# Optimization experiments

Hardware: AMD Instinct MI355X
Metric: run time of the kernel (lower is better)

The kernel has to match this reference:

```python
import jax, jax.numpy as jnp
import numpy as np

B, T, D, H, C = 128, 1000, 40, 128, 8  # batch, time, input feats, hidden, classes


def _lstm_layer(x, Wih, Whh, bih, bhh):
    """Unidirectional LSTM over time. x: [B,T,Din] -> [B,T,H]. PyTorch gate order i,f,g,o."""
    Bn = x.shape[0]
    Hn = Whh.shape[1]
    b = bih + bhh
    def step(carry, xt):
        h, c = carry
        g = xt @ Wih.T + h @ Whh.T + b  # [B,4H]
        i, f, gg, o = jnp.split(g, 4, axis=-1)
        c = jax.nn.sigmoid(f) * c + jax.nn.sigmoid(i) * jnp.tanh(gg)
        h = jax.nn.sigmoid(o) * jnp.tanh(c)
        return (h, c), h
    h0 = jnp.zeros((Bn, Hn), x.dtype)
    _, hs = jax.lax.scan(step, (h0, h0), jnp.swapaxes(x, 0, 1))  # scan over time
    return jnp.swapaxes(hs, 0, 1)


def _bilstm_layer(x, pf, pb):
    fwd = _lstm_layer(x, *pf)
    bwd = jnp.flip(_lstm_layer(jnp.flip(x, 1), *pb), 1)
    return jnp.concatenate([fwd, bwd], axis=-1)  # [B,T,2H]


def setup_inputs() -> dict:
    key = jax.random.key(0)
    ks = jax.random.split(key, 16)
    s = 0.05
    def rn(k, shape):
        return jax.random.normal(k, shape, jnp.float32) * s
    inp = {"x": jax.random.normal(ks[0], (B, T, D), jnp.float32)}
    inp["ln_g"] = jnp.ones((D,), jnp.float32)
    inp["ln_b"] = jnp.zeros((D,), jnp.float32)
    dims = [D, 2 * H]  # layer-0 input feats, layer-1 input feats
    i = 1
    for l in range(2):
        for d in ("f", "b"):
            inp[f"Wih_{d}{l}"] = rn(ks[i], (4 * H, dims[l])); i += 1
            inp[f"Whh_{d}{l}"] = rn(ks[i], (4 * H, H)); i += 1
            inp[f"bih_{d}{l}"] = jnp.zeros((4 * H,), jnp.float32)
            inp[f"bhh_{d}{l}"] = jnp.zeros((4 * H,), jnp.float32)
    inp["attn_W1"] = rn(ks[i], (H, 2 * H)); i += 1
    inp["attn_b1"] = jnp.zeros((H,), jnp.float32)
    inp["attn_w2"] = rn(ks[i], (1, H)); i += 1
    inp["fc_W1"] = rn(ks[i], (H, 2 * H)); i += 1
    inp["fc_b1"] = jnp.zeros((H,), jnp.float32)
    inp["fc_W2"] = rn(ks[i], (C, H)); i += 1
    inp["fc_b2"] = jnp.zeros((C,), jnp.float32)
    return inp


def reference(x, ln_g, ln_b,
              Wih_f0, Whh_f0, bih_f0, bhh_f0, Wih_b0, Whh_b0, bih_b0, bhh_b0,
              Wih_f1, Whh_f1, bih_f1, bhh_f1, Wih_b1, Whh_b1, bih_b1, bhh_b1,
              attn_W1, attn_b1, attn_w2, fc_W1, fc_b1, fc_W2, fc_b2):
    # LayerNorm over feature dim (eps=1e-5, PyTorch default)
    mu = jnp.mean(x, axis=-1, keepdims=True)
    var = jnp.var(x, axis=-1, keepdims=True)
    xn = (x - mu) * jax.lax.rsqrt(var + 1e-5) * ln_g + ln_b
    # 2-layer bidirectional LSTM
    h = _bilstm_layer(xn, (Wih_f0, Whh_f0, bih_f0, bhh_f0), (Wih_b0, Whh_b0, bih_b0, bhh_b0))
    h = _bilstm_layer(h, (Wih_f1, Whh_f1, bih_f1, bhh_f1), (Wih_b1, Whh_b1, bih_b1, bhh_b1))
    # attention pooling: Linear-Tanh-Linear(no bias) -> softmax over time
    scores = jnp.tanh(h @ attn_W1.T + attn_b1) @ attn_w2[0]  # [B,T]
    w = jax.nn.softmax(scores, axis=1)
    ctx = jnp.einsum('bt,btd->bd', w, h)  # [B,2H]
    # MLP classifier head
    hid = jax.nn.relu(ctx @ fc_W1.T + fc_b1)
    return hid @ fc_W2.T + fc_b2  # [B,C] logits
```

## Files before the change

### kernel.cpp

```cpp
#include <hip/hip_runtime.h>

#define T_ 1000

typedef float v2f __attribute__((ext_vector_type(2)));

__device__ __forceinline__ float sigf(float x) { return 1.0f / (1.0f + __expf(-x)); }
__device__ __forceinline__ float tanh_fast(float x) { return 1.0f - 2.0f / (1.0f + __expf(2.0f * x)); }
__device__ __forceinline__ float dot4(float4 a, float4 b) {
  return a.x * b.x + a.y * b.y + a.z * b.z + a.w * b.w;
}
__device__ __forceinline__ void pkfma(v2f& acc, float4 w, float4 v) {
  v2f wl; wl[0] = w.x; wl[1] = w.y;
  v2f wh; wh[0] = w.z; wh[1] = w.w;
  v2f vl; vl[0] = v.x; vl[1] = v.y;
  v2f vh; vh[0] = v.z; vh[1] = v.w;
  acc += wl * vl;
  acc += wh * vh;
}
__device__ __forceinline__ unsigned short f2bf(float f) {
  unsigned u = __float_as_uint(f);
  u = (u + 0x7fffu + ((u >> 16) & 1u)) >> 16;
  return (unsigned short)u;
}
__device__ __forceinline__ float bf2f(unsigned short h) {
  return __uint_as_float(((unsigned)h) << 16);
}
__device__ __forceinline__ float4 bf4_to_f4(ushort4 u) {
  float4 r;
  r.x = bf2f(u.x); r.y = bf2f(u.y); r.z = bf2f(u.z); r.w = bf2f(u.w);
  return r;
}

__global__ void bail_kernel(float* out, int n) {
  for (int i = threadIdx.x; i < n; i += 256) out[i] = 0.0f;
}

__global__ __launch_bounds__(256) void ln_stats_kernel(const float* __restrict__ x,
                                                       float* __restrict__ mu_arr,
                                                       float* __restrict__ rs_arr) {
  const int lane = threadIdx.x & 63;
  const int w = threadIdx.x >> 6;
  const long row = (long)blockIdx.x * 4 + w;
  float v = (lane < 40) ? x[row * 40 + lane] : 0.0f;
  float s1 = v, s2 = v * v;
  for (int m = 32; m; m >>= 1) {
    s1 += __shfl_xor(s1, m, 64);
    s2 += __shfl_xor(s2, m, 64);
  }
  if (lane == 0) {
    const float mu = s1 * (1.0f / 40.0f);
    const float var = s2 * (1.0f / 40.0f) - mu * mu;
    mu_arr[row] = mu;
    rs_arr[row] = rsqrtf(var + 1e-5f);
  }
}

__global__ __launch_bounds__(512, 1) void rec0_kernel(
    const float* __restrict__ x,
    const float* __restrict__ mu_arr, const float* __restrict__ rs_arr,
    const float* __restrict__ ln_g, const float* __restrict__ ln_b,
    const float* __restrict__ Wih_f, const float* __restrict__ Whh_f,
    const float* __restrict__ bih_f, const float* __restrict__ bhh_f,
    const float* __restrict__ Wih_b, const float* __restrict__ Whh_b,
    const float* __restrict__ bih_b, const float* __restrict__ bhh_b,
    float* __restrict__ h0) {
  const int tid = threadIdx.x;
  const int u = (tid >> 6) * 16 + ((tid & 63) >> 2);
  const int p = tid & 3;
  const int brow = blockIdx.x & 127;
  const int dir = blockIdx.x >> 7;
  const float* __restrict__ Wih = dir ? Wih_b : Wih_f;
  const float* __restrict__ Whh = dir ? Whh_b : Whh_f;
  const float* __restrict__ bih = dir ? bih_b : bih_f;
  const float* __restrict__ bhh = dir ? bhh_b : bhh_f;

  float4 wh[4][8];
  float4 wi[4][3];
  float S1[4], bias[4];
#pragma unroll
  for (int g = 0; g < 4; ++g) {
    const int row = g * 128 + u;
    const float4* wr = (const float4*)(Whh + row * 128 + p * 32);
#pragma unroll
    for (int ff = 0; ff < 8; ++ff) wh[g][ff] = wr[(ff + 2 * p) & 7];
    float s1p = 0.0f, s2p = 0.0f;
#pragma unroll
    for (int f = 0; f < 3; ++f) {
      float tmp[4];
#pragma unroll
      for (int e = 0; e < 4; ++e) {
        const int k = p * 12 + f * 4 + e;
        const float wv = (k < 40) ? Wih[row * 40 + k] : 0.0f;
        const float gk = (k < 40) ? ln_g[k] : 0.0f;
        const float bk = (k < 40) ? ln_b[k] : 0.0f;
        const float wf = wv * gk;
        tmp[e] = wf;
        s1p += wf;
        s2p += wv * bk;
      }
      wi[g][f] = make_float4(tmp[0], tmp[1], tmp[2], tmp[3]);
    }
    s1p += __shfl_xor(s1p, 1, 64); s1p += __shfl_xor(s1p, 2, 64);
    s2p += __shfl_xor(s2p, 1, 64); s2p += __shfl_xor(s2p, 2, 64);
    S1[g] = s1p;
    bias[g] = bih[g * 128 + u] + bhh[g * 128 + u] + s2p;
  }

  __shared__ float h4f[128];
  __shared__ __align__(16) float x_ring[2][8][48];
  __shared__ float mu_ring[2][8], rs_ring[2][8];
  __shared__ float hring[2][8][128];

  const int lr8 = tid / 40;
  const int lcol = tid - lr8 * 40;
  const long xbase = (long)brow * T_ * 40;
  const long mbase = (long)brow * T_;
  const long hbase = (long)brow * T_ * 256;

  if (tid < 128) h4f[tid] = 0.0f;
  if (tid < 128) {
    const int b = tid >> 6, r = (tid >> 3) & 7, cc = 40 + (tid & 7);
    x_ring[b][r][cc] = 0.0f;
  }
  if (tid < 320) {
    const int t = lr8;
    const int tt = dir ? (T_ - 1 - t) : t;
    x_ring[0][lr8][lcol] = x[xbase + (long)tt * 40 + lcol];
  } else if (tid < 328) {
    const int t = tid - 320;
    const int tt = dir ? (T_ - 1 - t) : t;
    mu_ring[0][t] = mu_arr[mbase + tt];
  } else if (tid < 336) {
    const int t = tid - 328;
    const int tt = dir ? (T_ - 1 - t) : t;
    rs_ring[0][t] = rs_arr[mbase + tt];
  }
  float c = 0.0f;
  float xpf = 0.0f, mupf = 0.0f, rspf = 0.0f;
  __syncthreads();

  for (int sb = 0; sb < 125; ++sb) {
    const int rb = sb & 1;
#pragma unroll
    for (int su = 0; su < 8; ++su) {
      if (su == 0) {
        if (sb + 1 < 125) {
          if (tid < 320) {
            const int t = (sb + 1) * 8 + lr8;
            const int tt = dir ? (T_ - 1 - t) : t;
            xpf = x[xbase + (long)tt * 40 + lcol];
          } else if (tid < 328) {
            const int t = (sb + 1) * 8 + (tid - 320);
            const int tt = dir ? (T_ - 1 - t) : t;
            mupf = mu_arr[mbase + tt];
          } else if (tid < 336) {
            const int t = (sb + 1) * 8 + (tid - 328);
            const int tt = dir ? (T_ - 1 - t) : t;
            rspf = rs_arr[mbase + tt];
          }
        }
        if (sb > 0) {
#pragma unroll
          for (int e = 0; e < 2; ++e) {
            const int idx = tid + e * 512;
            const int v = idx >> 7, j = idx & 127;
            const int ts = (sb - 1) * 8 + v;
            const int te = dir ? (T_ - 1 - ts) : ts;
            h0[hbase + (long)te * 256 + dir * 128 + j] = hring[rb ^ 1][v][j];
          }
        }
      }
      v2f hacc[4], xacc[4];
#pragma unroll
      for (int g = 0; g < 4; ++g) { hacc[g] = 0.0f; xacc[g] = 0.0f; }
      const float4* h4v = (const float4*)h4f;
#pragma unroll
      for (int ff = 0; ff < 8; ++ff) {
        const float4 hv = h4v[p * 8 + ((ff + 2 * p) & 7)];
        pkfma(hacc[0], wh[0][ff], hv);
        pkfma(hacc[1], wh[1][ff], hv);
        pkfma(hacc[2], wh[2][ff], hv);
        pkfma(hacc[3], wh[3][ff], hv);
      }
      const float4* xr4 = (const float4*)x_ring[rb][su];
#pragma unroll
      for (int f = 0; f < 3; ++f) {
        const float4 xv = xr4[p * 3 + f];
        pkfma(xacc[0], wi[0][f], xv);
        pkfma(xacc[1], wi[1][f], xv);
        pkfma(xacc[2], wi[2][f], xv);
        pkfma(xacc[3], wi[3][f], xv);
      }
      const float rs = rs_ring[rb][su];
      const float mu = mu_ring[rb][su];
      float pg[4];
#pragma unroll
      for (int g = 0; g < 4; ++g) {
        pg[g] = (hacc[g][0] + hacc[g][1]) + rs * (xacc[g][0] + xacc[g][1]);
        pg[g] += __shfl_xor(pg[g], 1, 64);
        pg[g] += __shfl_xor(pg[g], 2, 64);
        pg[g] += bias[g] - rs * mu * S1[g];
      }
      const float ig = sigf(pg[0]);
      const float fg = sigf(pg[1]);
      const float gg = tanh_fast(pg[2]);
      const float og = sigf(pg[3]);
      c = fg * c + ig * gg;
      const float hv = og * tanh_fast(c);
      if (p == 0) { h4f[u] = hv; hring[rb][su][u] = hv; }
      if (su == 7 && sb + 1 < 125) {
        if (tid < 320) x_ring[rb ^ 1][lr8][lcol] = xpf;
        else if (tid < 328) mu_ring[rb ^ 1][tid - 320] = mupf;
        else if (tid < 336) rs_ring[rb ^ 1][tid - 328] = rspf;
      }
      __syncthreads();
    }
  }
#pragma unroll
  for (int e = 0; e < 2; ++e) {
    const int idx = tid + e * 512;
    const int v = idx >> 7, j = idx & 127;
    const int ts = 124 * 8 + v;
    const int te = dir ? (T_ - 1 - ts) : ts;
    h0[hbase + (long)te * 256 + dir * 128 + j] = hring[0][v][j];
  }
}

__global__ __launch_bounds__(512, 1) void rec1_kernel(
    const float* __restrict__ xw_f, const float* __restrict__ xw_b,
    const float* __restrict__ Whh_f, const float* __restrict__ bih_f, const float* __restrict__ bhh_f,
    const float* __restrict__ Whh_b, const float* __restrict__ bih_b, const float* __restrict__ bhh_b,
    unsigned short* __restrict__ h1b, float* __restrict__ state,
    int Tc, int t0f, int t0b, int first) {
  const int tid = threadIdx.x;
  const int u = (tid >> 6) * 16 + ((tid & 63) >> 2);
  const int p = tid & 3;
  const int brow = blockIdx.x & 127;
  const int dir = blockIdx.x >> 7;
  const float* __restrict__ xw = dir ? xw_b : xw_f;
  const float* __restrict__ Whh = dir ? Whh_b : Whh_f;
  const float* __restrict__ bih = dir ? bih_b : bih_f;
  const float* __restrict__ bhh = dir ? bhh_b : bhh_f;
  const int t0 = dir ? t0b : t0f;

  float4 wh[4][8];
#pragma unroll
  for (int g = 0; g < 4; ++g) {
    const float4* wr = (const float4*)(Whh + (g * 128 + u) * 128 + p * 32);
#pragma unroll
    for (int ff = 0; ff < 8; ++ff) wh[g][ff] = wr[(ff + 2 * p) & 7];
  }
  const int myrow = p * 128 + u;
  const float bias_p = bih[myrow] + bhh[myrow];

  __shared__ float h4f[128];
  __shared__ float hring[2][8][128];
  float* sblk = state + (long)blockIdx.x * 256;
  float c = 0.0f;
  if (first) {
    if (tid < 128) h4f[tid] = 0.0f;
  } else {
    if (tid < 128) h4f[tid] = sblk[tid];
    c = sblk[128 + u];
  }
  const long gbase = (long)brow * Tc;
  float xr[8];
#pragma unroll
  for (int v = 0; v < 8; ++v) {
    xr[v] = 0.0f;
    if (v < Tc) {
      const int tr = dir ? (Tc - 1 - v) : v;
      xr[v] = xw[(gbase + tr) * 512 + myrow];
    }
  }
  __syncthreads();

  const int nSB = (Tc + 7) / 8;
  for (int sb = 0; sb < nSB; ++sb) {
    const int rb = sb & 1;
#pragma unroll
    for (int su = 0; su < 8; ++su) {
      const int s = sb * 8 + su;
      if (s >= Tc) break;
      if (su == 0 && sb > 0) {
#pragma unroll
        for (int e = 0; e < 2; ++e) {
          const int idx = tid + e * 512;
          const int v = idx >> 7, j = idx & 127;
          const int s2 = (sb - 1) * 8 + v;
          const int tt = dir ? (Tc - 1 - s2) : s2;
          h1b[((long)brow * T_ + (t0 + tt)) * 256 + dir * 128 + j] = f2bf(hring[rb ^ 1][v][j]);
        }
      }
      v2f hacc[4];
#pragma unroll
      for (int g = 0; g < 4; ++g) hacc[g] = 0.0f;
      const float4* h4v = (const float4*)h4f;
#pragma unroll
      for (int ff = 0; ff < 8; ++ff) {
        const float4 hv = h4v[p * 8 + ((ff + 2 * p) & 7)];
        pkfma(hacc[0], wh[0][ff], hv);
        pkfma(hacc[1], wh[1][ff], hv);
        pkfma(hacc[2], wh[2][ff], hv);
        pkfma(hacc[3], wh[3][ff], hv);
      }
      const float xin = xr[su] + bias_p;
      float pg[4];
#pragma unroll
      for (int g = 0; g < 4; ++g) {
        pg[g] = hacc[g][0] + hacc[g][1] + ((p == g) ? xin : 0.0f);
        pg[g] += __shfl_xor(pg[g], 1, 64);
        pg[g] += __shfl_xor(pg[g], 2, 64);
      }
      const float ig = sigf(pg[0]);
      const float fg = sigf(pg[1]);
      const float gg = tanh_fast(pg[2]);
      const float og = sigf(pg[3]);
      c = fg * c + ig * gg;
      const float hv = og * tanh_fast(c);
      if (p == 0) { h4f[u] = hv; hring[rb][su][u] = hv; }
      if (su == 7) {
#pragma unroll
        for (int v = 0; v < 8; ++v) {
          const int sn = s + 1 + v;
          xr[v] = 0.0f;
          if (sn < Tc) {
            const int tr = dir ? (Tc - 1 - sn) : sn;
            xr[v] = xw[(gbase + tr) * 512 + myrow];
          }
        }
      }
      __syncthreads();
    }
  }
  {
    const int sbL = (Tc - 1) >> 3;
    const int cnt = Tc - sbL * 8;
    const int rbL = sbL & 1;
#pragma unroll
    for (int e = 0; e < 2; ++e) {
      const int idx = tid + e * 512;
      const int v = idx >> 7, j = idx & 127;
      if (v < cnt) {
        const int s2 = sbL * 8 + v;
        const int tt = dir ? (Tc - 1 - s2) : s2;
        h1b[((long)brow * T_ + (t0 + tt)) * 256 + dir * 128 + j] = f2bf(hring[rbL][v][j]);
      }
    }
  }
  if (tid < 128) sblk[tid] = h4f[tid];
  if (p == 0) sblk[128 + u] = c;
}

__global__ __launch_bounds__(256, 2) void gemm_xw1(
    const float* __restrict__ h0,
    const float* __restrict__ Wf, const float* __restrict__ Wb,
    float* __restrict__ xwf, float* __restrict__ xwb,
    int Tc, int t0f, int t0b) {
  __shared__ float As[64 * 36];
  __shared__ float Bs[128 * 36];
  __shared__ int rowbase[64];
  const int tid = threadIdx.x;
  const int tx = tid & 15, ty = tid >> 4;
  const int r0 = blockIdx.x * 64;
  const int jt = blockIdx.y;
  const int dir = jt >> 2;
  const int nh = jt & 3;
  const float* __restrict__ W = dir ? Wb : Wf;
  float* __restrict__ out = dir ? xwb : xwf;
  const int jbase = nh * 128;
  const int t0 = dir ? t0b : t0f;

  if (tid < 64) {
    const int r = r0 + tid;
    const int br = r / Tc;
    rowbase[tid] = br * T_ + t0 + (r - br * Tc);
  }

  float4* As4 = (float4*)As;
  float4* Bs4 = (float4*)Bs;
  v2f acc2[4][8];
#pragma unroll
  for (int r = 0; r < 4; ++r)
#pragma unroll
    for (int c2 = 0; c2 < 8; ++c2) acc2[r][c2] = 0.0f;
#pragma unroll 1
  for (int kk = 0; kk < 8; ++kk) {
    __syncthreads();
#pragma unroll
    for (int i = 0; i < 2; ++i) {
      const int q = tid + i * 256;
      const int row = q >> 3, k4 = q & 7;
      As4[row * 9 + k4] = *(const float4*)&h0[(long)rowbase[row] * 256 + kk * 32 + k4 * 4];
    }
#pragma unroll
    for (int i = 0; i < 4; ++i) {
      const int q = tid + i * 256;
      const int row = q >> 3, k4 = q & 7;
      Bs4[row * 9 + k4] = *(const float4*)&W[(long)(jbase + row) * 256 + kk * 32 + k4 * 4];
    }
    __syncthreads();
#pragma unroll 1
    for (int k4 = 0; k4 < 8; ++k4) {
      float4 av[4];
#pragma unroll
      for (int r = 0; r < 4; ++r) av[r] = As4[(ty * 4 + r) * 9 + k4];
#pragma unroll
      for (int c2 = 0; c2 < 8; ++c2) {
        const float4 bv = Bs4[(tx + 16 * c2) * 9 + k4];
#pragma unroll
        for (int r = 0; r < 4; ++r) pkfma(acc2[r][c2], av[r], bv);
      }
    }
  }
#pragma unroll
  for (int r = 0; r < 4; ++r) {
    const long ob = (long)(r0 + ty * 4 + r) * 512 + jbase + tx;
#pragma unroll
    for (int c2 = 0; c2 < 8; ++c2) out[ob + c2 * 16] = acc2[r][c2][0] + acc2[r][c2][1];
  }
}

__global__ __launch_bounds__(256, 2) void score_kernel(
    const unsigned short* __restrict__ h1b, const float* __restrict__ W1,
    const float* __restrict__ b1, const float* __restrict__ w2,
    float* __restrict__ scores) {
  __shared__ float As[64 * 36];
  __shared__ float Bs[128 * 36];
  const int tid = threadIdx.x;
  const int tx = tid & 15, ty = tid >> 4;
  const long r0 = (long)blockIdx.x * 64;

  float4* As4 = (float4*)As;
  float4* Bs4 = (float4*)Bs;
  v2f acc2[4][8];
#pragma unroll
  for (int r = 0; r < 4; ++r)
#pragma unroll
    for (int c2 = 0; c2 < 8; ++c2) acc2[r][c2] = 0.0f;
#pragma unroll 1
  for (int kk = 0; kk < 8; ++kk) {
    __syncthreads();
#pragma unroll
    for (int i = 0; i < 2; ++i) {
      const int q = tid + i * 256;
      const int row = q >> 3, k4 = q & 7;
      const ushort4 uv = *(const ushort4*)&h1b[(r0 + row) * 256 + kk * 32 + k4 * 4];
      As4[row * 9 + k4] = bf4_to_f4(uv);
    }
#pragma unroll
    for (int i = 0; i < 4; ++i) {
      const int q = tid + i * 256;
      const int row = q >> 3, k4 = q & 7;
      Bs4[row * 9 + k4] = *(const float4*)&W1[(long)row * 256 + kk * 32 + k4 * 4];
    }
    __syncthreads();
#pragma unroll 1
    for (int k4 = 0; k4 < 8; ++k4) {
      float4 av[4];
#pragma unroll
      for (int r = 0; r < 4; ++r) av[r] = As4[(ty * 4 + r) * 9 + k4];
#pragma unroll
      for (int c2 = 0; c2 < 8; ++c2) {
        const float4 bv = Bs4[(tx + 16 * c2) * 9 + k4];
#pragma unroll
        for (int r = 0; r < 4; ++r) pkfma(acc2[r][c2], av[r], bv);
      }
    }
  }
#pragma unroll
  for (int r = 0; r < 4; ++r) {
    float s = 0.0f;
#pragma unroll
    for (int c2 = 0; c2 < 8; ++c2) {
      const int col = tx + 16 * c2;
      s += tanh_fast(acc2[r][c2][0] + acc2[r][c2][1] + b1[col]) * w2[col];
    }
#pragma unroll
    for (int m = 1; m < 16; m <<= 1) s += __shfl_xor(s, m, 16);
    if (tx == 0) scores[r0 + ty * 4 + r] = s;
  }
}

__global__ __launch_bounds__(256, 2) void head_kernel(
    const float* __restrict__ scores, const unsigned short* __restrict__ h1b,
    const float* __restrict__ fW1, const float* __restrict__ fb1,
    const float* __restrict__ fW2, const float* __restrict__ fb2,
    float* __restrict__ outp) {
  const int b = blockIdx.x, tid = threadIdx.x;
  __shared__ float wls[1000];
  __shared__ float red[8];
  __shared__ __align__(16) float ctx[256];
  __shared__ __align__(16) float hid[128];

  float sv[4];
  float mx = -1e30f;
#pragma unroll
  for (int i = 0; i < 4; ++i) {
    const int t = tid + i * 256;
    sv[i] = (t < 1000) ? scores[b * 1000 + t] : -1e30f;
    mx = fmaxf(mx, sv[i]);
  }
  for (int m = 32; m; m >>= 1) mx = fmaxf(mx, __shfl_xor(mx, m, 64));
  if ((tid & 63) == 0) red[tid >> 6] = mx;
  __syncthreads();
  mx = fmaxf(fmaxf(red[0], red[1]), fmaxf(red[2], red[3]));
  float se = 0.0f;
#pragma unroll
  for (int i = 0; i < 4; ++i) {
    const int t = tid + i * 256;
    if (t < 1000) {
      const float e = __expf(sv[i] - mx);
      wls[t] = e;
      se += e;
    }
  }
  for (int m = 32; m; m >>= 1) se += __shfl_xor(se, m, 64);
  if ((tid & 63) == 0) red[4 + (tid >> 6)] = se;
  __syncthreads();
  const float rinv = 1.0f / (red[4] + red[5] + red[6] + red[7]);

  float a = 0.0f;
  const unsigned short* hb = h1b + (long)b * T_ * 256 + tid;
  for (int t = 0; t < T_; ++t) a = fmaf(wls[t], bf2f(hb[t * 256]), a);
  ctx[tid] = a * rinv;
  __syncthreads();
  if (tid < 128) {
    float s = fb1[tid];
    const float4* wr = (const float4*)&fW1[tid * 256];
    const float4* cc = (const float4*)ctx;
#pragma unroll
    for (int f = 0; f < 64; ++f) s += dot4(wr[f], cc[f]);
    hid[tid] = fmaxf(s, 0.0f);
  }
  __syncthreads();
  if (tid < 8) {
    float s = fb2[tid];
    const float4* wr = (const float4*)&fW2[tid * 128];
    const float4* hh = (const float4*)hid;
#pragma unroll
    for (int f = 0; f < 32; ++f) s += dot4(wr[f], hh[f]);
    outp[b * 8 + tid] = s;
  }
}

extern "C" void kernel_launch(void* const* d_in, const int* in_sizes, int n_in,
                              void* d_out, int out_size, void* d_ws, size_t ws_size,
                              hipStream_t stream) {
  (void)in_sizes; (void)n_in; (void)out_size;
  const float* x       = (const float*)d_in[0];
  const float* ln_g    = (const float*)d_in[1];
  const float* ln_b    = (const float*)d_in[2];
  const float* Wih_f0  = (const float*)d_in[3];
  const float* Whh_f0  = (const float*)d_in[4];
  const float* bih_f0  = (const float*)d_in[5];
  const float* bhh_f0  = (const float*)d_in[6];
  const float* Wih_b0  = (const float*)d_in[7];
  const float* Whh_b0  = (const float*)d_in[8];
  const float* bih_b0  = (const float*)d_in[9];
  const float* bhh_b0  = (const float*)d_in[10];
  const float* Wih_f1  = (const float*)d_in[11];
  const float* Whh_f1  = (const float*)d_in[12];
  const float* bih_f1  = (const float*)d_in[13];
  const float* bhh_f1  = (const float*)d_in[14];
  const float* Wih_b1  = (const float*)d_in[15];
  const float* Whh_b1  = (const float*)d_in[16];
  const float* bih_b1  = (const float*)d_in[17];
  const float* bhh_b1  = (const float*)d_in[18];
  const float* attn_W1 = (const float*)d_in[19];
  const float* attn_b1 = (const float*)d_in[20];
  const float* attn_w2 = (const float*)d_in[21];
  const float* fc_W1   = (const float*)d_in[22];
  const float* fc_b1   = (const float*)d_in[23];
  const float* fc_W2   = (const float*)d_in[24];
  const float* fc_b2   = (const float*)d_in[25];

  char* base = (char*)d_ws;
  size_t off = 0;
  auto alloc = [&](size_t bytes) {
    char* ptr = base + off;
    off += (bytes + 255) & ~(size_t)255;
    return ptr;
  };
  float*          h0    = (float*)alloc(32768000ull * 4);
  unsigned short* h1b   = (unsigned short*)alloc(32768000ull * 2);
  float*          state = (float*)alloc(65536ull * 4);
  float*          scor  = (float*)alloc(128000ull * 4);
  float*          mu_a  = (float*)alloc(128000ull * 4);
  float*          rs_a  = (float*)alloc(128000ull * 4);

  const size_t rem = (ws_size > off) ? (ws_size - off) : 0;
  static const int cands[16] = {1000, 500, 250, 200, 125, 100, 50, 40, 25, 20, 10, 8, 5, 4, 2, 1};
  int Tc = 0;
  for (int ci = 0; ci < 16; ++ci) {
    if (524288ull * (size_t)cands[ci] <= rem) { Tc = cands[ci]; break; }
  }
  if (Tc == 0) {
    bail_kernel<<<dim3(1), dim3(256), 0, stream>>>((float*)d_out, 1024);
    return;
  }
  float* xwf = (float*)(base + off);
  float* xwb = xwf + 65536L * Tc;

  ln_stats_kernel<<<dim3(32000), dim3(256), 0, stream>>>(x, mu_a, rs_a);
  rec0_kernel<<<dim3(256), dim3(512), 0, stream>>>(x, mu_a, rs_a, ln_g, ln_b,
                                                   Wih_f0, Whh_f0, bih_f0, bhh_f0,
                                                   Wih_b0, Whh_b0, bih_b0, bhh_b0, h0);
  const int nch = T_ / Tc;
  for (int ch = 0; ch < nch; ++ch) {
    const int t0f = ch * Tc;
    const int t0b = T_ - (ch + 1) * Tc;
    gemm_xw1<<<dim3(2 * Tc, 8), dim3(256), 0, stream>>>(h0, Wih_f1, Wih_b1, xwf, xwb, Tc, t0f, t0b);
    rec1_kernel<<<dim3(256), dim3(512), 0, stream>>>(xwf, xwb, Whh_f1, bih_f1, bhh_f1,
                                                     Whh_b1, bih_b1, bhh_b1, h1b, state,
                                                     Tc, t0f, t0b, (ch == 0) ? 1 : 0);
  }
  score_kernel<<<dim3(2000), dim3(256), 0, stream>>>(h1b, attn_W1, attn_b1, attn_w2, scor);
  head_kernel<<<dim3(128), dim3(256), 0, stream>>>(scor, h1b, fc_W1, fc_b1, fc_W2, fc_b2,
                                                   (float*)d_out);
}
```

Before: 2.887 ms.

## Double-buffer recurrent hidden state, set waves_per_eu, revert GEMM packed FMA

Both recurrent kernels now keep the shared hidden-state vector in two buffers, alternating by step parity. This removes the hazard between reading the old h and writing the new h within a step, which could allow fewer barriers later. The launch bounds become amdgpu_waves_per_eu(2,2), which changes the register budget and allowed occupancy. The projection and score GEMMs go back from packed v2f FMA to scalar dot4 accumulation, which uses fewer accumulator registers but drops packed math.

```diff
diff --git a/kernel.cpp b/kernel.cpp
--- a/kernel.cpp
+++ b/kernel.cpp
@@ -55,7 +55,7 @@
   }
 }
 
-__global__ __launch_bounds__(512, 1) void rec0_kernel(
+__global__ __launch_bounds__(512) __attribute__((amdgpu_waves_per_eu(2, 2))) void rec0_kernel(
     const float* __restrict__ x,
     const float* __restrict__ mu_arr, const float* __restrict__ rs_arr,
     const float* __restrict__ ln_g, const float* __restrict__ ln_b,
@@ -106,7 +106,7 @@
     bias[g] = bih[g * 128 + u] + bhh[g * 128 + u] + s2p;
   }
 
-  __shared__ float h4f[128];
+  __shared__ float h4f[2][128];
   __shared__ __align__(16) float x_ring[2][8][48];
   __shared__ float mu_ring[2][8], rs_ring[2][8];
   __shared__ float hring[2][8][128];
@@ -117,7 +117,7 @@
   const long mbase = (long)brow * T_;
   const long hbase = (long)brow * T_ * 256;
 
-  if (tid < 128) h4f[tid] = 0.0f;
+  if (tid < 128) h4f[0][tid] = 0.0f;
   if (tid < 128) {
     const int b = tid >> 6, r = (tid >> 3) & 7, cc = 40 + (tid & 7);
     x_ring[b][r][cc] = 0.0f;
@@ -143,6 +143,7 @@
     const int rb = sb & 1;
 #pragma unroll
     for (int su = 0; su < 8; ++su) {
+      const int rdq = su & 1, wrq = rdq ^ 1;
       if (su == 0) {
         if (sb + 1 < 125) {
           if (tid < 320) {
@@ -173,7 +174,7 @@
       v2f hacc[4], xacc[4];
 #pragma unroll
       for (int g = 0; g < 4; ++g) { hacc[g] = 0.0f; xacc[g] = 0.0f; }
-      const float4* h4v = (const float4*)h4f;
+      const float4* h4v = (const float4*)h4f[rdq];
 #pragma unroll
       for (int ff = 0; ff < 8; ++ff) {
         const float4 hv = h4v[p * 8 + ((ff + 2 * p) & 7)];
@@ -207,7 +208,7 @@
       const float og = sigf(pg[3]);
       c = fg * c + ig * gg;
       const float hv = og * tanh_fast(c);
-      if (p == 0) { h4f[u] = hv; hring[rb][su][u] = hv; }
+      if (p == 0) { h4f[wrq][u] = hv; hring[rb][su][u] = hv; }
       if (su == 7 && sb + 1 < 125) {
         if (tid < 320) x_ring[rb ^ 1][lr8][lcol] = xpf;
         else if (tid < 328) mu_ring[rb ^ 1][tid - 320] = mupf;
@@ -226,7 +227,7 @@
   }
 }
 
-__global__ __launch_bounds__(512, 1) void rec1_kernel(
+__global__ __launch_bounds__(512) __attribute__((amdgpu_waves_per_eu(2, 2))) void rec1_kernel(
     const float* __restrict__ xw_f, const float* __restrict__ xw_b,
     const float* __restrict__ Whh_f, const float* __restrict__ bih_f, const float* __restrict__ bhh_f,
     const float* __restrict__ Whh_b, const float* __restrict__ bih_b, const float* __restrict__ bhh_b,
@@ -253,14 +254,14 @@
   const int myrow = p * 128 + u;
   const float bias_p = bih[myrow] + bhh[myrow];
 
-  __shared__ float h4f[128];
+  __shared__ float h4f[2][128];
   __shared__ float hring[2][8][128];
   float* sblk = state + (long)blockIdx.x * 256;
   float c = 0.0f;
   if (first) {
-    if (tid < 128) h4f[tid] = 0.0f;
+    if (tid < 128) h4f[0][tid] = 0.0f;
   } else {
-    if (tid < 128) h4f[tid] = sblk[tid];
+    if (tid < 128) h4f[0][tid] = sblk[tid];
     c = sblk[128 + u];
   }
   const long gbase = (long)brow * Tc;
@@ -282,6 +283,7 @@
     for (int su = 0; su < 8; ++su) {
       const int s = sb * 8 + su;
       if (s >= Tc) break;
+      const int rdq = su & 1, wrq = rdq ^ 1;
       if (su == 0 && sb > 0) {
 #pragma unroll
         for (int e = 0; e < 2; ++e) {
@@ -295,7 +297,7 @@
       v2f hacc[4];
 #pragma unroll
       for (int g = 0; g < 4; ++g) hacc[g] = 0.0f;
-      const float4* h4v = (const float4*)h4f;
+      const float4* h4v = (const float4*)h4f[rdq];
 #pragma unroll
       for (int ff = 0; ff < 8; ++ff) {
         const float4 hv = h4v[p * 8 + ((ff + 2 * p) & 7)];
@@ -318,7 +320,7 @@
       const float og = sigf(pg[3]);
       c = fg * c + ig * gg;
       const float hv = og * tanh_fast(c);
-      if (p == 0) { h4f[u] = hv; hring[rb][su][u] = hv; }
+      if (p == 0) { h4f[wrq][u] = hv; hring[rb][su][u] = hv; }
       if (su == 7) {
 #pragma unroll
         for (int v = 0; v < 8; ++v) {
@@ -348,7 +350,7 @@
       }
     }
   }
-  if (tid < 128) sblk[tid] = h4f[tid];
+  if (tid < 128) sblk[tid] = h4f[Tc & 1][tid];
   if (p == 0) sblk[128 + u] = c;
 }
 
@@ -379,11 +381,7 @@
 
   float4* As4 = (float4*)As;
   float4* Bs4 = (float4*)Bs;
-  v2f acc2[4][8];
-#pragma unroll
-  for (int r = 0; r < 4; ++r)
-#pragma unroll
-    for (int c2 = 0; c2 < 8; ++c2) acc2[r][c2] = 0.0f;
+  float acc[4][8] = {};
 #pragma unroll 1
   for (int kk = 0; kk < 8; ++kk) {
     __syncthreads();
@@ -409,7 +407,7 @@
       for (int c2 = 0; c2 < 8; ++c2) {
         const float4 bv = Bs4[(tx + 16 * c2) * 9 + k4];
 #pragma unroll
-        for (int r = 0; r < 4; ++r) pkfma(acc2[r][c2], av[r], bv);
+        for (int r = 0; r < 4; ++r) acc[r][c2] += dot4(av[r], bv);
       }
     }
   }
@@ -417,7 +415,7 @@
   for (int r = 0; r < 4; ++r) {
     const long ob = (long)(r0 + ty * 4 + r) * 512 + jbase + tx;
 #pragma unroll
-    for (int c2 = 0; c2 < 8; ++c2) out[ob + c2 * 16] = acc2[r][c2][0] + acc2[r][c2][1];
+    for (int c2 = 0; c2 < 8; ++c2) out[ob + c2 * 16] = acc[r][c2];
   }
 }
 
@@ -433,11 +431,7 @@
 
   float4* As4 = (float4*)As;
   float4* Bs4 = (float4*)Bs;
-  v2f acc2[4][8];
-#pragma unroll
-  for (int r = 0; r < 4; ++r)
-#pragma unroll
-    for (int c2 = 0; c2 < 8; ++c2) acc2[r][c2] = 0.0f;
+  float acc[4][8] = {};
 #pragma unroll 1
   for (int kk = 0; kk < 8; ++kk) {
     __syncthreads();
@@ -464,7 +458,7 @@
       for (int c2 = 0; c2 < 8; ++c2) {
         const float4 bv = Bs4[(tx + 16 * c2) * 9 + k4];
 #pragma unroll
-        for (int r = 0; r < 4; ++r) pkfma(acc2[r][c2], av[r], bv);
+        for (int r = 0; r < 4; ++r) acc[r][c2] += dot4(av[r], bv);
       }
     }
   }
@@ -474,7 +468,7 @@
 #pragma unroll
     for (int c2 = 0; c2 < 8; ++c2) {
       const int col = tx + 16 * c2;
-      s += tanh_fast(acc2[r][c2][0] + acc2[r][c2][1] + b1[col]) * w2[col];
+      s += tanh_fast(acc[r][c2] + b1[col]) * w2[col];
     }
 #pragma unroll
     for (int m = 1; m < 16; m <<= 1) s += __shfl_xor(s, m, 16);
```

Result: slower. 3.173 ms (+9.9%).
